# Performance work log

Measured on AMD Instinct MI355X. Metric: run time of the kernel, lower is better.

The kernel has to match this reference:

```python
import jax, jax.numpy as jnp
import numpy as np

ALPHA = 0.2  # LeakyReLU negative slope


def _gat_layer(x, xq, src, dst, W_l, a_l, N):
    # x, xq: [N, Din]; W_l: [Din, D]; a_l: [2*D]
    h = x @ W_l            # [N, D]
    hq = xq @ W_l          # [N, D]
    D = W_l.shape[1]
    # a @ cat(hq[src], h[dst]) splits into two per-node dot products
    sq = hq @ a_l[:D]      # [N]
    sn = h @ a_l[D:]       # [N]
    s = sq[src] + sn[dst]  # [E]
    e = jnp.exp(-jnp.where(s >= 0, s, ALPHA * s))          # [E]
    rowsum = jax.ops.segment_sum(e, src, num_segments=N)    # [N]
    agg = jax.ops.segment_sum(e[:, None] * h[dst], src, num_segments=N)  # [N, D]
    denom = jnp.where(rowsum == 0, 1.0, rowsum)[:, None]
    h_prime = agg / denom
    # torch replaces NaN (0/0) with 0; isolated nodes -> 0
    return jnp.where(rowsum[:, None] == 0, 0.0, h_prime)


def setup_inputs() -> dict:
    key = jax.random.key(0)
    k1, k2, k3, k4, k5 = jax.random.split(key, 5)
    B, N, D, E, L = 2, 20000, 256, 320000, 2
    nodes = jax.random.normal(k1, (B, N, D), dtype=jnp.float32)
    nodes_query = jax.random.normal(k2, (B, N, D), dtype=jnp.float32)
    W = jax.random.normal(k3, (L, D, D), dtype=jnp.float32) * 0.088  # xavier_normal gain=1.414
    a = jax.random.normal(k4, (L, 2 * D), dtype=jnp.float32) * 0.074
    edges = jax.random.randint(k5, (B, 2, E), 0, N, dtype=jnp.int32)
    return {"nodes": nodes, "nodes_query": nodes_query, "W": W, "a": a, "edges": edges}


def reference(nodes, nodes_query, W, a, edges):
    B, N, D = nodes.shape
    L = W.shape[0]

    def per_graph(x, xq, e):
        src, dst = e[0], e[1]
        h = x
        for l in range(L):  # small fixed layer count
            h = _gat_layer(h, xq, src, dst, W[l], a[l], N)
        return h

    out = jax.vmap(per_graph)(nodes, nodes_query, edges)
    return out + nodes  # residual
```

## Files before the change

### kernel.cpp

```cpp
#include <hip/hip_runtime.h>
#include <hip/hip_fp16.h>
#include <math.h>

constexpr int N = 20000, D = 256, E = 320000, B = 2, L = 2;
constexpr int CAP = 64;

typedef _Float16 f16x8 __attribute__((ext_vector_type(8)));
typedef float f32x4 __attribute__((ext_vector_type(4)));

__device__ __forceinline__ unsigned short f2h(float f) {
  __half h = __float2half(f);
  return *(unsigned short*)&h;
}
__device__ __forceinline__ float2 h2f(unsigned int u) {
  __half2 hv = *reinterpret_cast<__half2*>(&u);
  return __half22float2(hv);
}

__global__ __launch_bounds__(256) void prep_kernel(const float* __restrict__ W,
                                                   const float* __restrict__ a,
                                                   unsigned short* __restrict__ Wt,
                                                   float* __restrict__ wa,
                                                   uint4* __restrict__ zbase) {
  int bi = blockIdx.x, tid = threadIdx.x;
  if (bi < 512) {
    __shared__ float t[16][17];
    int l = bi >> 8, rem = bi & 255;
    int by = rem >> 4, bx = rem & 15;
    int tx = tid & 15, ty = tid >> 4;
    t[ty][tx] = W[l * 65536 + (by * 16 + ty) * 256 + bx * 16 + tx];
    __syncthreads();
    Wt[l * 65536 + (bx * 16 + ty) * 256 + by * 16 + tx] = f2h(t[tx][ty]);
  } else if (bi < 514) {
    int l = bi - 512;
    float s = 0.f;
    for (int d = 0; d < D; ++d) s += W[l * 65536 + tid * D + d] * a[l * 2 * D + d];
    wa[l * D + tid] = s;
  } else {
    int zi = (bi - 514) * 256 + tid;
    if (zi < 10000) zbase[zi] = make_uint4(0, 0, 0, 0);
  }
}

template <bool F32A>
__device__ __forceinline__ void gemm_body(const void* __restrict__ Av,
                                          const unsigned short* __restrict__ Wt,
                                          unsigned short* __restrict__ Ch,
                                          const float* __restrict__ a2,
                                          float* __restrict__ snp, int M, int z, int bm, int bn,
                                          int tid) {
  __shared__ unsigned short As[128 * 32];
  __shared__ unsigned short Bs[64 * 32];
  unsigned short* Cz = Ch + (size_t)z * M * 256;
  float* snz = snp + (size_t)z * M * 4;
  int q = bn >> 6;
  int wv = tid >> 6, lane = tid & 63;
  int lm = lane & 15, lq = lane >> 4;
  f32x4 acc[2][4] = {};

  for (int k0 = 0; k0 < 256; k0 += 32) {
    int m = tid >> 1, kb = (tid & 1) << 4;
    if (bm + m < M) {
      if constexpr (F32A) {
        const float* ap = (const float*)Av + (size_t)z * M * 256 + (size_t)(bm + m) * 256 + k0 + kb;
        float4 v0 = ((const float4*)ap)[0];
        float4 v1 = ((const float4*)ap)[1];
        float4 v2 = ((const float4*)ap)[2];
        float4 v3 = ((const float4*)ap)[3];
        unsigned short t[16] = {f2h(v0.x), f2h(v0.y), f2h(v0.z), f2h(v0.w),
                                f2h(v1.x), f2h(v1.y), f2h(v1.z), f2h(v1.w),
                                f2h(v2.x), f2h(v2.y), f2h(v2.z), f2h(v2.w),
                                f2h(v3.x), f2h(v3.y), f2h(v3.z), f2h(v3.w)};
        *(uint4*)&As[m * 32 + kb] = *(uint4*)t;
        *(uint4*)&As[m * 32 + kb + 8] = *(uint4*)(t + 8);
      } else {
        const unsigned short* ap =
            (const unsigned short*)Av + (size_t)z * M * 256 + (size_t)(bm + m) * 256 + k0 + kb;
        *(uint4*)&As[m * 32 + kb] = *(const uint4*)ap;
        *(uint4*)&As[m * 32 + kb + 8] = *(const uint4*)(ap + 8);
      }
    } else {
      uint4 z4 = make_uint4(0, 0, 0, 0);
      *(uint4*)&As[m * 32 + kb] = z4;
      *(uint4*)&As[m * 32 + kb + 8] = z4;
    }
    int nn = tid >> 2, kb2 = (tid & 3) << 3;
    *(uint4*)&Bs[nn * 32 + kb2] = *(const uint4*)(Wt + (size_t)(bn + nn) * 256 + k0 + kb2);
    __syncthreads();

    f16x8 af0 = *(const f16x8*)&As[(wv * 32 + lm) * 32 + lq * 8];
    f16x8 af1 = *(const f16x8*)&As[(wv * 32 + 16 + lm) * 32 + lq * 8];
#pragma unroll
    for (int nf = 0; nf < 4; ++nf) {
      f16x8 bfr = *(const f16x8*)&Bs[(nf * 16 + lm) * 32 + lq * 8];
      acc[0][nf] = __builtin_amdgcn_mfma_f32_16x16x32_f16(af0, bfr, acc[0][nf], 0, 0, 0);
      acc[1][nf] = __builtin_amdgcn_mfma_f32_16x16x32_f16(af1, bfr, acc[1][nf], 0, 0, 0);
    }
    __syncthreads();
  }

  float a2v[4];
#pragma unroll
  for (int nf = 0; nf < 4; ++nf) a2v[nf] = a2[bn + nf * 16 + lm];
#pragma unroll
  for (int f = 0; f < 2; ++f) {
#pragma unroll
    for (int r = 0; r < 4; ++r) {
      int row = bm + wv * 32 + f * 16 + lq * 4 + r;
      if (row < M) {
        float partial = 0.f;
#pragma unroll
        for (int nf = 0; nf < 4; ++nf) {
          float v = acc[f][nf][r];
          Cz[(size_t)row * 256 + bn + nf * 16 + lm] = f2h(v);
          partial += v * a2v[nf];
        }
        partial += __shfl_xor(partial, 1);
        partial += __shfl_xor(partial, 2);
        partial += __shfl_xor(partial, 4);
        partial += __shfl_xor(partial, 8);
        if (lm == 0) snz[((size_t)row << 2) | q] = partial;
      }
    }
  }
}

__global__ __launch_bounds__(256) void mega0_kernel(const float* __restrict__ nodes,
                                                    const unsigned short* __restrict__ Wt,
                                                    unsigned short* __restrict__ hhf,
                                                    const float* __restrict__ a2l0,
                                                    float* __restrict__ sn0,
                                                    const float* __restrict__ xq,
                                                    const float* __restrict__ wa,
                                                    float* __restrict__ sq,
                                                    const int* __restrict__ edges,
                                                    int* __restrict__ deg,
                                                    int* __restrict__ slot) {
  int bi = blockIdx.x, tid = threadIdx.x;
  if (bi < 625) {
    int ebase = bi * 1024 + tid;
    int s4[4], d4[4];
#pragma unroll
    for (int q = 0; q < 4; ++q) {
      int e = ebase + q * 256;
      int b = (e >= E) ? 1 : 0;
      s4[q] = edges[(size_t)b * E + e];
      d4[q] = edges[(size_t)(b + 1) * E + e];
    }
#pragma unroll
    for (int q = 0; q < 4; ++q) {
      int e = ebase + q * 256;
      int b = (e >= E) ? 1 : 0;
      int nb = b * N + s4[q];
      int pos = atomicAdd(&deg[nb], 1);
      if (pos < CAP) slot[((size_t)nb << 6) + pos] = d4[q];
    }
  } else if (bi < 1881) {
    int g = bi - 625;
    int z = g / 628;
    int rem = g % 628;
    int bm = (rem >> 2) * 128;
    int bn = (rem & 3) * 64;
    gemm_body<true>(nodes, Wt, hhf, a2l0, sn0, N, z, bm, bn, tid);
  } else {
    int sqb = bi - 1881;
    int b = (sqb >= 5000) ? 1 : 0;
    int blk = sqb - b * 5000;
    int wave = blk * 4 + (tid >> 6);
    int lane = tid & 63;
    const float4 xv = *(const float4*)(xq + ((size_t)b * N + wave) * D + (lane << 2));
    const float4 w0 = *(const float4*)(wa + (lane << 2));
    const float4 w1 = *(const float4*)(wa + D + (lane << 2));
    float s0 = xv.x * w0.x + xv.y * w0.y + xv.z * w0.z + xv.w * w0.w;
    float s1 = xv.x * w1.x + xv.y * w1.y + xv.z * w1.z + xv.w * w1.w;
    for (int off = 32; off; off >>= 1) {
      s0 += __shfl_down(s0, off);
      s1 += __shfl_down(s1, off);
    }
    if (lane == 0) {
      sq[(b * 2 + 0) * N + wave] = s0;
      sq[(b * 2 + 1) * N + wave] = s1;
    }
  }
}

__global__ __launch_bounds__(256) void gemm_l1(const unsigned short* __restrict__ A,
                                               const unsigned short* __restrict__ Wt,
                                               unsigned short* __restrict__ Ch,
                                               const float* __restrict__ a2,
                                               float* __restrict__ sn, int M) {
  gemm_body<false>(A, Wt, Ch, a2, sn, M, blockIdx.z, blockIdx.y * 128, blockIdx.x * 64,
                   threadIdx.x);
}

__global__ __launch_bounds__(256) void agg_kernel(const int* __restrict__ deg,
                                                  const int* __restrict__ slot,
                                                  const float* __restrict__ sq_all,
                                                  const float* __restrict__ snp,
                                                  const unsigned short* __restrict__ hhf,
                                                  const float* __restrict__ resid,
                                                  float* __restrict__ outf,
                                                  unsigned short* __restrict__ outh, int l) {
  int b = blockIdx.y;
  int tid = threadIdx.x, wv = tid >> 6, lane = tid & 63;
  int node = blockIdx.x * 4 + wv;
  int eg = lane >> 5, dl = lane & 31;
  const float4* snb = (const float4*)snp + (size_t)b * N;
  const unsigned short* hb = hhf + (size_t)b * N * 256;
  int nb = b * N + node;
  int cnt = min(deg[nb], CAP);
  const int* sl = slot + ((size_t)nb << 6);
  float sqv = sq_all[((b << 1) + l) * N + node];
  int key = (lane < cnt) ? sl[lane] : 0x7fffffff;
#pragma unroll
  for (int k = 2; k <= 64; k <<= 1) {
#pragma unroll
    for (int j = k >> 1; j > 0; j >>= 1) {
      int o = __shfl_xor(key, j);
      bool keepMin = (((lane & k) == 0) == ((lane & j) == 0));
      key = keepMin ? min(key, o) : max(key, o);
    }
  }
  int idx = (lane < cnt) ? key : 0;
  float snv = 0.f;
  if (lane < cnt) {
    float4 sv = snb[idx];
    snv = (sv.x + sv.y) + (sv.z + sv.w);
  }
  int nj = (cnt - eg + 1) >> 1;
  uint4 hv[4];
#pragma unroll
  for (int u = 0; u < 4; ++u) {
    int dsti = __shfl(idx, eg + 2 * u);
    if (u < nj) hv[u] = *(const uint4*)(hb + (size_t)dsti * 256 + (dl << 3));
  }
  float s = sqv + snv;
  float lr = (s >= 0.f) ? s : 0.2f * s;
  float w = (lane < cnt) ? __expf(-lr) : 0.f;
  float wsum = w;
  float acc[8] = {};
  for (int u0 = 0; u0 < nj; u0 += 4) {
    uint4 hn[4];
#pragma unroll
    for (int u = 0; u < 4; ++u) {
      int uu = u0 + 4 + u;
      int js = eg + 2 * uu;
      js = (js < 63) ? js : 63;
      int dsti = __shfl(idx, js);
      if (uu < nj) hn[u] = *(const uint4*)(hb + (size_t)dsti * 256 + (dl << 3));
    }
#pragma unroll
    for (int u = 0; u < 4; ++u) {
      int uu = u0 + u;
      if (uu < nj) {
        float wj = __shfl(w, eg + 2 * uu);
        float2 f0 = h2f(hv[u].x), f1 = h2f(hv[u].y), f2 = h2f(hv[u].z), f3 = h2f(hv[u].w);
        acc[0] = fmaf(wj, f0.x, acc[0]);
        acc[1] = fmaf(wj, f0.y, acc[1]);
        acc[2] = fmaf(wj, f1.x, acc[2]);
        acc[3] = fmaf(wj, f1.y, acc[3]);
        acc[4] = fmaf(wj, f2.x, acc[4]);
        acc[5] = fmaf(wj, f2.y, acc[5]);
        acc[6] = fmaf(wj, f3.x, acc[6]);
        acc[7] = fmaf(wj, f3.y, acc[7]);
      }
    }
#pragma unroll
    for (int u = 0; u < 4; ++u) hv[u] = hn[u];
  }
  for (int off = 32; off; off >>= 1) wsum += __shfl_xor(wsum, off);
#pragma unroll
  for (int i = 0; i < 8; ++i) acc[i] += __shfl_xor(acc[i], 32);
  float inv = (wsum > 0.f) ? 1.f / wsum : 0.f;
  float o0 = (eg ? acc[4] : acc[0]) * inv;
  float o1 = (eg ? acc[5] : acc[1]) * inv;
  float o2 = (eg ? acc[6] : acc[2]) * inv;
  float o3 = (eg ? acc[7] : acc[3]) * inv;
  size_t rowoff = ((size_t)b * N + node) * 256 + (dl << 3) + (eg << 2);
  if (outh) {
    unsigned short t[4] = {f2h(o0), f2h(o1), f2h(o2), f2h(o3)};
    *(uint2*)(outh + rowoff) = *(uint2*)t;
  } else {
    const float4 rv = *(const float4*)(resid + rowoff);
    *(float4*)(outf + rowoff) = make_float4(o0 + rv.x, o1 + rv.y, o2 + rv.z, o3 + rv.w);
  }
}

extern "C" void kernel_launch(void* const* d_in, const int* in_sizes, int n_in,
                              void* d_out, int out_size, void* d_ws, size_t ws_size,
                              hipStream_t stream) {
  const float* nodes = (const float*)d_in[0];
  const float* nodesq = (const float*)d_in[1];
  const float* W = (const float*)d_in[2];
  const float* a = (const float*)d_in[3];
  const int* edges = (const int*)d_in[4];
  float* out = (float*)d_out;

  const size_t ND = (size_t)N * D;
  unsigned short* hhf = (unsigned short*)d_ws;
  unsigned short* h1hf = hhf + (size_t)B * ND;
  unsigned short* Wt = h1hf + (size_t)B * ND;
  int* deg = (int*)(Wt + (size_t)L * D * D);
  float* sn0 = (float*)(deg + B * N);
  float* sn1 = sn0 + (size_t)B * N * 4;
  float* sq_all = sn1 + (size_t)B * N * 4;
  float* wa = sq_all + (size_t)B * L * N;
  int* slot = (int*)(wa + L * D);

  prep_kernel<<<554, 256, 0, stream>>>(W, a, Wt, wa, (uint4*)deg);
  mega0_kernel<<<11881, 256, 0, stream>>>(nodes, Wt, hhf, a + D, sn0, nodesq, wa, sq_all,
                                          edges, deg, slot);
  agg_kernel<<<dim3(N / 4, B), 256, 0, stream>>>(deg, slot, sq_all, sn0, hhf, nullptr,
                                                 nullptr, h1hf, 0);
  gemm_l1<<<dim3(4, (N + 127) / 128, B), 256, 0, stream>>>(h1hf, Wt + (size_t)D * D, hhf,
                                                           a + 3 * D, sn1, N);
  agg_kernel<<<dim3(N / 4, B), 256, 0, stream>>>(deg, slot, sq_all, sn1, hhf, nodes, out,
                                                 nullptr, 1);
}
```

Before: 296.2 us.

## Shard edge bucketing by source range, shrink slot indices to u16, pad LDS rows

The edge-bucketing phase now runs as 8 shards. Each shard re-reads all edges but handles only sources in its own 5000-node range, which keeps the atomics and slot writes local to a smaller footprint. Slot entries are stored as 16-bit indices instead of 32-bit, halving slot memory traffic in bucketing and aggregation. GEMM shared-memory rows are padded from 32 to 40 halves to reduce LDS bank conflicts. The cost is 8x redundant edge reads and a much larger grid.

After: 291.5 us. About the same (-1.6%).

```diff
diff --git a/kernel.cpp b/kernel.cpp
--- a/kernel.cpp
+++ b/kernel.cpp
@@ -4,6 +4,7 @@
 
 constexpr int N = 20000, D = 256, E = 320000, B = 2, L = 2;
 constexpr int CAP = 64;
+constexpr int LDA = 40;
 
 typedef _Float16 f16x8 __attribute__((ext_vector_type(8)));
 typedef float f32x4 __attribute__((ext_vector_type(4)));
@@ -49,8 +50,8 @@
                                           const float* __restrict__ a2,
                                           float* __restrict__ snp, int M, int z, int bm, int bn,
                                           int tid) {
-  __shared__ unsigned short As[128 * 32];
-  __shared__ unsigned short Bs[64 * 32];
+  __shared__ unsigned short As[128 * LDA];
+  __shared__ unsigned short Bs[64 * LDA];
   unsigned short* Cz = Ch + (size_t)z * M * 256;
   float* snz = snp + (size_t)z * M * 4;
   int q = bn >> 6;
@@ -71,28 +72,28 @@
                                 f2h(v1.x), f2h(v1.y), f2h(v1.z), f2h(v1.w),
                                 f2h(v2.x), f2h(v2.y), f2h(v2.z), f2h(v2.w),
                                 f2h(v3.x), f2h(v3.y), f2h(v3.z), f2h(v3.w)};
-        *(uint4*)&As[m * 32 + kb] = *(uint4*)t;
-        *(uint4*)&As[m * 32 + kb + 8] = *(uint4*)(t + 8);
+        *(uint4*)&As[m * LDA + kb] = *(uint4*)t;
+        *(uint4*)&As[m * LDA + kb + 8] = *(uint4*)(t + 8);
       } else {
         const unsigned short* ap =
             (const unsigned short*)Av + (size_t)z * M * 256 + (size_t)(bm + m) * 256 + k0 + kb;
-        *(uint4*)&As[m * 32 + kb] = *(const uint4*)ap;
-        *(uint4*)&As[m * 32 + kb + 8] = *(const uint4*)(ap + 8);
+        *(uint4*)&As[m * LDA + kb] = *(const uint4*)ap;
+        *(uint4*)&As[m * LDA + kb + 8] = *(const uint4*)(ap + 8);
       }
     } else {
       uint4 z4 = make_uint4(0, 0, 0, 0);
-      *(uint4*)&As[m * 32 + kb] = z4;
-      *(uint4*)&As[m * 32 + kb + 8] = z4;
+      *(uint4*)&As[m * LDA + kb] = z4;
+      *(uint4*)&As[m * LDA + kb + 8] = z4;
     }
     int nn = tid >> 2, kb2 = (tid & 3) << 3;
-    *(uint4*)&Bs[nn * 32 + kb2] = *(const uint4*)(Wt + (size_t)(bn + nn) * 256 + k0 + kb2);
+    *(uint4*)&Bs[nn * LDA + kb2] = *(const uint4*)(Wt + (size_t)(bn + nn) * 256 + k0 + kb2);
     __syncthreads();
 
-    f16x8 af0 = *(const f16x8*)&As[(wv * 32 + lm) * 32 + lq * 8];
-    f16x8 af1 = *(const f16x8*)&As[(wv * 32 + 16 + lm) * 32 + lq * 8];
+    f16x8 af0 = *(const f16x8*)&As[(wv * 32 + lm) * LDA + lq * 8];
+    f16x8 af1 = *(const f16x8*)&As[(wv * 32 + 16 + lm) * LDA + lq * 8];
 #pragma unroll
     for (int nf = 0; nf < 4; ++nf) {
-      f16x8 bfr = *(const f16x8*)&Bs[(nf * 16 + lm) * 32 + lq * 8];
+      f16x8 bfr = *(const f16x8*)&Bs[(nf * 16 + lm) * LDA + lq * 8];
       acc[0][nf] = __builtin_amdgcn_mfma_f32_16x16x32_f16(af0, bfr, acc[0][nf], 0, 0, 0);
       acc[1][nf] = __builtin_amdgcn_mfma_f32_16x16x32_f16(af1, bfr, acc[1][nf], 0, 0, 0);
     }
@@ -135,35 +136,33 @@
                                                     float* __restrict__ sq,
                                                     const int* __restrict__ edges,
                                                     int* __restrict__ deg,
-                                                    int* __restrict__ slot) {
+                                                    unsigned short* __restrict__ slot) {
   int bi = blockIdx.x, tid = threadIdx.x;
-  if (bi < 625) {
-    int ebase = bi * 1024 + tid;
-    int s4[4], d4[4];
-#pragma unroll
-    for (int q = 0; q < 4; ++q) {
-      int e = ebase + q * 256;
+  if (bi < 5000) {
+    int shard = bi & 7, slice = bi >> 3;
+    int lo = shard * 5000;
+    int ebase = slice * 1024 + tid;
+#pragma unroll
+    for (int qq = 0; qq < 4; ++qq) {
+      int e = ebase + qq * 256;
       int b = (e >= E) ? 1 : 0;
-      s4[q] = edges[(size_t)b * E + e];
-      d4[q] = edges[(size_t)(b + 1) * E + e];
-    }
-#pragma unroll
-    for (int q = 0; q < 4; ++q) {
-      int e = ebase + q * 256;
-      int b = (e >= E) ? 1 : 0;
-      int nb = b * N + s4[q];
-      int pos = atomicAdd(&deg[nb], 1);
-      if (pos < CAP) slot[((size_t)nb << 6) + pos] = d4[q];
-    }
-  } else if (bi < 1881) {
-    int g = bi - 625;
+      int s = edges[(size_t)b * E + e];
+      int d = edges[(size_t)(b + 1) * E + e];
+      int nb = b * N + s;
+      if ((unsigned)(nb - lo) < 5000u) {
+        int pos = atomicAdd(&deg[nb], 1);
+        if (pos < CAP) slot[((size_t)nb << 6) + pos] = (unsigned short)d;
+      }
+    }
+  } else if (bi < 6256) {
+    int g = bi - 5000;
     int z = g / 628;
     int rem = g % 628;
     int bm = (rem >> 2) * 128;
     int bn = (rem & 3) * 64;
     gemm_body<true>(nodes, Wt, hhf, a2l0, sn0, N, z, bm, bn, tid);
   } else {
-    int sqb = bi - 1881;
+    int sqb = bi - 6256;
     int b = (sqb >= 5000) ? 1 : 0;
     int blk = sqb - b * 5000;
     int wave = blk * 4 + (tid >> 6);
@@ -194,7 +193,7 @@
 }
 
 __global__ __launch_bounds__(256) void agg_kernel(const int* __restrict__ deg,
-                                                  const int* __restrict__ slot,
+                                                  const unsigned short* __restrict__ slot,
                                                   const float* __restrict__ sq_all,
                                                   const float* __restrict__ snp,
                                                   const unsigned short* __restrict__ hhf,
@@ -209,9 +208,9 @@
   const unsigned short* hb = hhf + (size_t)b * N * 256;
   int nb = b * N + node;
   int cnt = min(deg[nb], CAP);
-  const int* sl = slot + ((size_t)nb << 6);
+  const unsigned short* sl = slot + ((size_t)nb << 6);
   float sqv = sq_all[((b << 1) + l) * N + node];
-  int key = (lane < cnt) ? sl[lane] : 0x7fffffff;
+  int key = (lane < cnt) ? (int)sl[lane] : 0x7fffffff;
 #pragma unroll
   for (int k = 2; k <= 64; k <<= 1) {
 #pragma unroll
@@ -305,10 +304,10 @@
   float* sn1 = sn0 + (size_t)B * N * 4;
   float* sq_all = sn1 + (size_t)B * N * 4;
   float* wa = sq_all + (size_t)B * L * N;
-  int* slot = (int*)(wa + L * D);
+  unsigned short* slot = (unsigned short*)(wa + L * D);
 
   prep_kernel<<<554, 256, 0, stream>>>(W, a, Wt, wa, (uint4*)deg);
-  mega0_kernel<<<11881, 256, 0, stream>>>(nodes, Wt, hhf, a + D, sn0, nodesq, wa, sq_all,
+  mega0_kernel<<<16256, 256, 0, stream>>>(nodes, Wt, hhf, a + D, sn0, nodesq, wa, sq_all,
                                           edges, deg, slot);
   agg_kernel<<<dim3(N / 4, B), 256, 0, stream>>>(deg, slot, sq_all, sn0, hhf, nullptr,
                                                  nullptr, h1hf, 0);
```
